# Kernel tuning notes

Measured on AMD Instinct MI355X. Metric: run time of the kernel, lower is better.

The kernel has to match this reference:

```python
import jax, jax.numpy as jnp
import numpy as np

B, T, D = 4, 2048, 1024
E, F, K = 8, 4096, 2  # num experts, ffn hidden, top-k


def setup_inputs() -> dict:
    key = jax.random.key(0)
    ks = jax.random.split(key, 7)
    s_in = 1.0 / np.sqrt(D)
    s_ff = 1.0 / np.sqrt(F)
    return {
        "x": jax.random.normal(ks[0], (B, T, D), dtype=jnp.float32),
        "Wg": jax.random.normal(ks[1], (D, E), dtype=jnp.float32) * s_in,
        "bg": jnp.zeros((E,), dtype=jnp.float32),
        "W1": jax.random.normal(ks[2], (E, D, F), dtype=jnp.float32) * s_in,
        "b1": jnp.zeros((E, F), dtype=jnp.float32),
        "W2": jax.random.normal(ks[3], (E, F, D), dtype=jnp.float32) * s_ff,
        "b2": jnp.zeros((E, D), dtype=jnp.float32),
    }


def reference(x, Wg, bg, W1, b1, W2, b2):
    # Gate: per-token expert logits [B, T, E]
    logits = jnp.einsum("btd,de->bte", x, Wg) + bg
    # Top-k per token, softmax over only the selected logits (as in the source)
    topv, topi = jax.lax.top_k(logits, K)          # [B, T, K]
    probs = jax.nn.softmax(topv, axis=-1)           # [B, T, K]
    out = jnp.zeros_like(x)
    # Loop over the small fixed expert set; each expert runs a dense MLP over
    # all tokens, masked/weighted by its routing probability (0 if unselected).
    for e in range(E):
        w = jnp.sum(probs * (topi == e), axis=-1)   # [B, T] combine weight
        h = jax.nn.gelu(jnp.einsum("btd,df->btf", x, W1[e]) + b1[e], approximate=False)
        y = jnp.einsum("btf,fd->btd", h, W2[e]) + b2[e]
        out = out + w[..., None] * y
    return out
```

## Files before the change

### kernel.cpp

```cpp
#include <hip/hip_runtime.h>
#include <cstdint>

#define B_ 4
#define T_ 2048
#define D_ 1024
#define E_ 8
#define F_ 4096
#define K_ 2
#define N_ (B_*T_)
#define NR_ (N_*K_)

#define TM 128
#define BK 64
#define MAXP (NR_ + E_*TM)
#define MAXMB (NR_/TM + E_)

typedef __attribute__((ext_vector_type(8))) short short8;
typedef __attribute__((ext_vector_type(4))) float f32x4;

typedef const __attribute__((address_space(1))) unsigned int* gp1_t;
typedef __attribute__((address_space(3))) unsigned int* lp3_t;

__device__ __forceinline__ void gl_lds16(const void* g, void* l) {
    __builtin_amdgcn_global_load_lds((gp1_t)g, (lp3_t)l, 16, 0, 0);
}

__device__ __forceinline__ unsigned short f2b(float f) {
    union { float f; unsigned int u; } v; v.f = f;
    unsigned int u = v.u;
    return (unsigned short)((u + 0x7FFFu + ((u >> 16) & 1u)) >> 16);
}

__device__ __forceinline__ float b2f(unsigned short u) {
    union { unsigned int i; float f; } v; v.i = ((unsigned int)u) << 16;
    return v.f;
}

__device__ __forceinline__ float gelu_exact(float x) {
    return 0.5f * x * (1.0f + erff(x * 0.70710678118654752440f));
}

__global__ __launch_bounds__(256) void gate_kernel(
    const float* __restrict__ x, const float* __restrict__ Wg,
    const float* __restrict__ bg, int* __restrict__ topi,
    float* __restrict__ topw, int* __restrict__ counts) {
    int tid  = threadIdx.x;
    int lane = tid & 63;
    int tok  = blockIdx.x * 4 + (tid >> 6);
    int e = lane & 7;
    int c = lane >> 3;
    const float4* xp = (const float4*)(x + (size_t)tok * D_ + c * 128);
    const float*  wp = Wg + (size_t)(c * 128) * E_ + e;
    float acc = 0.f;
    #pragma unroll 8
    for (int i = 0; i < 32; ++i) {
        float4 xv = xp[i];
        acc += xv.x * wp[(i*4+0)*E_];
        acc += xv.y * wp[(i*4+1)*E_];
        acc += xv.z * wp[(i*4+2)*E_];
        acc += xv.w * wp[(i*4+3)*E_];
    }
    acc += __shfl_xor(acc, 8, 64);
    acc += __shfl_xor(acc, 16, 64);
    acc += __shfl_xor(acc, 32, 64);
    float logit = acc + bg[e];
    float v1 = -3.4e38f, v2 = -3.4e38f; int i1 = -1, i2 = -1;
    for (int ee = 0; ee < 8; ++ee) {
        float le = __shfl(logit, ee, 64);
        if (le > v1) { v2 = v1; i2 = i1; v1 = le; i1 = ee; }
        else if (le > v2) { v2 = le; i2 = ee; }
    }
    if (lane == 0) {
        float p2 = expf(v2 - v1);
        float s  = 1.0f + p2;
        topi[tok*2]   = i1; topw[tok*2]   = 1.0f / s;
        topi[tok*2+1] = i2; topw[tok*2+1] = p2 / s;
        atomicAdd(&counts[i1], 1);
        atomicAdd(&counts[i2], 1);
    }
}

__global__ void scan_kernel(const int* __restrict__ counts,
                            int* __restrict__ offs, int* __restrict__ cursors,
                            int* __restrict__ mb_e, int* __restrict__ mb_m0) {
    if (threadIdx.x == 0) {
        int s = 0, mb = 0;
        for (int e = 0; e < E_; ++e) {
            offs[e] = s; cursors[e] = s;
            int nb = (counts[e] + TM - 1) / TM;
            for (int i = 0; i < nb; ++i) { mb_e[mb] = e; mb_m0[mb] = s + i*TM; ++mb; }
            s += nb * TM;
        }
        offs[E_] = s;
        for (int b = mb; b < MAXMB; ++b) mb_e[b] = -1;
    }
}

__global__ __launch_bounds__(256) void scatter_kernel(
    const int* __restrict__ topi, int* __restrict__ cursors,
    int* __restrict__ perm, int* __restrict__ slots) {
    int t = blockIdx.x * blockDim.x + threadIdx.x;
    if (t >= N_) return;
    #pragma unroll
    for (int k = 0; k < K_; ++k) {
        int e = topi[t*2 + k];
        int pos = atomicAdd(&cursors[e], 1);
        perm[pos] = t;
        slots[t*2 + k] = pos;
    }
}

__global__ __launch_bounds__(256) void castx_kernel(
    const float* __restrict__ x, unsigned short* __restrict__ xb) {
    int i = blockIdx.x * blockDim.x + threadIdx.x;
    float4 v = ((const float4*)x)[i];
    ushort4 o; o.x = f2b(v.x); o.y = f2b(v.y); o.z = f2b(v.z); o.w = f2b(v.w);
    ((ushort4*)xb)[i] = o;
}

__global__ __launch_bounds__(256) void tcast_kernel(
    const float* __restrict__ src, unsigned short* __restrict__ dst, int R, int C) {
    __shared__ float tile[64][65];
    int rb = blockIdx.x * 64, cb = blockIdx.y * 64;
    const float* s = src + (size_t)blockIdx.z * R * C;
    unsigned short* d = dst + (size_t)blockIdx.z * R * C;
    int tx = threadIdx.x & 15, ty = threadIdx.x >> 4;
    #pragma unroll
    for (int i = 0; i < 4; ++i) {
        int r = ty + i*16;
        float4 v = *(const float4*)&s[(size_t)(rb + r) * C + cb + tx*4];
        tile[r][tx*4+0] = v.x; tile[r][tx*4+1] = v.y;
        tile[r][tx*4+2] = v.z; tile[r][tx*4+3] = v.w;
    }
    __syncthreads();
    #pragma unroll
    for (int i = 0; i < 4; ++i) {
        int c = ty + i*16;
        ushort4 o;
        o.x = f2b(tile[tx*4+0][c]);
        o.y = f2b(tile[tx*4+1][c]);
        o.z = f2b(tile[tx*4+2][c]);
        o.w = f2b(tile[tx*4+3][c]);
        *(ushort4*)&d[(size_t)(cb + c) * R + rb + tx*4] = o;
    }
}

__global__ __launch_bounds__(256, 4) void ffn1_kernel(
    const unsigned short* __restrict__ Xb, const unsigned short* __restrict__ W1t,
    const float* __restrict__ b1, const int* __restrict__ perm,
    const int* __restrict__ mb_e, const int* __restrict__ mb_m0,
    unsigned short* __restrict__ H) {
    int e = mb_e[blockIdx.x];
    if (e < 0) return;
    int m0 = mb_m0[blockIdx.x];
    int n0 = blockIdx.y * 128;
    const unsigned short* Bw = W1t + (size_t)e * F_ * D_;

    __shared__ __align__(16) unsigned short lA[128*BK];
    __shared__ __align__(16) unsigned short lB[128*BK];

    int t = threadIdx.x;
    int lane = t & 63;
    int wv = t >> 6;
    int wrow = (wv >> 1) * 64, wcol = (wv & 1) * 64;
    int lr = lane & 15, q = lane >> 4;
    int xork = lr & 7;

    int sr = t >> 3;
    int sc = ((t & 7) ^ (sr & 7)) * 8;
    const unsigned short* pa[4];
    const unsigned short* pb[4];
    #pragma unroll
    for (int i = 0; i < 4; ++i) {
        int tok = perm[m0 + sr + 32*i];
        pa[i] = Xb + (size_t)tok * D_ + sc;
        pb[i] = Bw + (size_t)(n0 + sr + 32*i) * D_ + sc;
    }

    f32x4 acc[4][4];
    #pragma unroll
    for (int mi = 0; mi < 4; ++mi)
        #pragma unroll
        for (int ni = 0; ni < 4; ++ni)
            acc[mi][ni] = (f32x4){0.f, 0.f, 0.f, 0.f};

    for (int kk = 0; kk < D_/BK; ++kk) {
        int k0 = kk * BK;
        #pragma unroll
        for (int i = 0; i < 4; ++i) {
            gl_lds16(pa[i] + k0, &lA[i*2048 + t*8]);
            gl_lds16(pb[i] + k0, &lB[i*2048 + t*8]);
        }
        asm volatile("s_waitcnt vmcnt(0)" ::: "memory");
        __syncthreads();
        #pragma unroll
        for (int s = 0; s < 2; ++s) {
            short8 af[4], bf[4];
            #pragma unroll
            for (int mi = 0; mi < 4; ++mi)
                af[mi] = *(const short8*)&lA[(wrow + mi*16 + lr)*BK + (((s*4+q) ^ xork) * 8)];
            #pragma unroll
            for (int ni = 0; ni < 4; ++ni)
                bf[ni] = *(const short8*)&lB[(wcol + ni*16 + lr)*BK + (((s*4+q) ^ xork) * 8)];
            #pragma unroll
            for (int mi = 0; mi < 4; ++mi)
                #pragma unroll
                for (int ni = 0; ni < 4; ++ni)
                    acc[mi][ni] = __builtin_amdgcn_mfma_f32_16x16x32_bf16(
                        af[mi], bf[ni], acc[mi][ni], 0, 0, 0);
        }
        __syncthreads();
    }

    const float* b1e = b1 + (size_t)e * F_;
    #pragma unroll
    for (int mi = 0; mi < 4; ++mi) {
        int gr = m0 + wrow + mi*16 + q*4;
        #pragma unroll
        for (int ni = 0; ni < 4; ++ni) {
            int f = n0 + wcol + ni*16 + lr;
            float bb = b1e[f];
            #pragma unroll
            for (int r = 0; r < 4; ++r) {
                float h = gelu_exact(acc[mi][ni][r] + bb);
                H[(size_t)(gr + r) * F_ + f] = f2b(h);
            }
        }
    }
}

__global__ __launch_bounds__(256, 4) void ffn2_kernel(
    const unsigned short* __restrict__ H, const unsigned short* __restrict__ W2t,
    const float* __restrict__ b2,
    const int* __restrict__ mb_e, const int* __restrict__ mb_m0,
    unsigned short* __restrict__ Y) {
    int e = mb_e[blockIdx.x];
    if (e < 0) return;
    int m0 = mb_m0[blockIdx.x];
    int n0 = blockIdx.y * 128;
    const unsigned short* Bw = W2t + (size_t)e * D_ * F_;

    __shared__ __align__(16) unsigned short lA[128*BK];
    __shared__ __align__(16) unsigned short lB[128*BK];

    int t = threadIdx.x;
    int lane = t & 63;
    int wv = t >> 6;
    int wrow = (wv >> 1) * 64, wcol = (wv & 1) * 64;
    int lr = lane & 15, q = lane >> 4;
    int xork = lr & 7;

    int sr = t >> 3;
    int sc = ((t & 7) ^ (sr & 7)) * 8;
    const unsigned short* pa[4];
    const unsigned short* pb[4];
    #pragma unroll
    for (int i = 0; i < 4; ++i) {
        pa[i] = H  + (size_t)(m0 + sr + 32*i) * F_ + sc;
        pb[i] = Bw + (size_t)(n0 + sr + 32*i) * F_ + sc;
    }

    f32x4 acc[4][4];
    #pragma unroll
    for (int mi = 0; mi < 4; ++mi)
        #pragma unroll
        for (int ni = 0; ni < 4; ++ni)
            acc[mi][ni] = (f32x4){0.f, 0.f, 0.f, 0.f};

    for (int kk = 0; kk < F_/BK; ++kk) {
        int k0 = kk * BK;
        #pragma unroll
        for (int i = 0; i < 4; ++i) {
            gl_lds16(pa[i] + k0, &lA[i*2048 + t*8]);
            gl_lds16(pb[i] + k0, &lB[i*2048 + t*8]);
        }
        asm volatile("s_waitcnt vmcnt(0)" ::: "memory");
        __syncthreads();
        #pragma unroll
        for (int s = 0; s < 2; ++s) {
            short8 af[4], bf[4];
            #pragma unroll
            for (int mi = 0; mi < 4; ++mi)
                af[mi] = *(const short8*)&lA[(wrow + mi*16 + lr)*BK + (((s*4+q) ^ xork) * 8)];
            #pragma unroll
            for (int ni = 0; ni < 4; ++ni)
                bf[ni] = *(const short8*)&lB[(wcol + ni*16 + lr)*BK + (((s*4+q) ^ xork) * 8)];
            #pragma unroll
            for (int mi = 0; mi < 4; ++mi)
                #pragma unroll
                for (int ni = 0; ni < 4; ++ni)
                    acc[mi][ni] = __builtin_amdgcn_mfma_f32_16x16x32_bf16(
                        af[mi], bf[ni], acc[mi][ni], 0, 0, 0);
        }
        __syncthreads();
    }

    const float* b2e = b2 + (size_t)e * D_;
    #pragma unroll
    for (int mi = 0; mi < 4; ++mi) {
        int gr = m0 + wrow + mi*16 + q*4;
        #pragma unroll
        for (int ni = 0; ni < 4; ++ni) {
            int dcol = n0 + wcol + ni*16 + lr;
            float bb = b2e[dcol];
            #pragma unroll
            for (int r = 0; r < 4; ++r)
                Y[(size_t)(gr + r) * D_ + dcol] = f2b(acc[mi][ni][r] + bb);
        }
    }
}

__global__ __launch_bounds__(256) void combine_kernel(
    const unsigned short* __restrict__ Y, const int* __restrict__ slots,
    const float* __restrict__ topw, float* __restrict__ out) {
    int t  = blockIdx.x;
    int d4 = threadIdx.x * 4;
    int s0 = slots[t*2], s1 = slots[t*2+1];
    float w0 = topw[t*2], w1 = topw[t*2+1];
    ushort4 y0 = *(const ushort4*)&Y[(size_t)s0 * D_ + d4];
    ushort4 y1 = *(const ushort4*)&Y[(size_t)s1 * D_ + d4];
    float4 o;
    o.x = w0*b2f(y0.x) + w1*b2f(y1.x);
    o.y = w0*b2f(y0.y) + w1*b2f(y1.y);
    o.z = w0*b2f(y0.z) + w1*b2f(y1.z);
    o.w = w0*b2f(y0.w) + w1*b2f(y1.w);
    *(float4*)&out[(size_t)t * D_ + d4] = o;
}

extern "C" void kernel_launch(void* const* d_in, const int* in_sizes, int n_in,
                              void* d_out, int out_size, void* d_ws, size_t ws_size,
                              hipStream_t stream) {
    const float* x  = (const float*)d_in[0];
    const float* Wg = (const float*)d_in[1];
    const float* bg = (const float*)d_in[2];
    const float* W1 = (const float*)d_in[3];
    const float* b1 = (const float*)d_in[4];
    const float* W2 = (const float*)d_in[5];
    const float* b2 = (const float*)d_in[6];
    float* out = (float*)d_out;

    char* wsp = (char*)d_ws;
    size_t off = 0;
    auto alloc = [&](size_t bytes) {
        void* p = wsp + off;
        off += (bytes + 255) & ~(size_t)255;
        return p;
    };
    int*   topi    = (int*)  alloc((size_t)NR_*4);
    float* topw    = (float*)alloc((size_t)NR_*4);
    int*   slots   = (int*)  alloc((size_t)NR_*4);
    int*   counts  = (int*)  alloc(E_*4);
    int*   offs    = (int*)  alloc((E_+1)*4);
    int*   cursors = (int*)  alloc(E_*4);
    int*   mb_e    = (int*)  alloc(MAXMB*4);
    int*   mb_m0   = (int*)  alloc(MAXMB*4);
    int*   perm    = (int*)  alloc((size_t)MAXP*4);
    unsigned short* Xb  = (unsigned short*)alloc((size_t)N_*D_*2);
    unsigned short* W1t = (unsigned short*)alloc((size_t)E_*D_*F_*2);
    unsigned short* W2t = (unsigned short*)alloc((size_t)E_*D_*F_*2);
    unsigned short* Hb  = (unsigned short*)alloc((size_t)MAXP*F_*2);
    unsigned short* Yb  = (unsigned short*)alloc((size_t)MAXP*D_*2);

    hipMemsetAsync(counts, 0, E_*4, stream);
    hipMemsetAsync(perm, 0, (size_t)MAXP*4, stream);

    gate_kernel<<<N_/4, 256, 0, stream>>>(x, Wg, bg, topi, topw, counts);
    scan_kernel<<<1, 64, 0, stream>>>(counts, offs, cursors, mb_e, mb_m0);
    scatter_kernel<<<N_/256, 256, 0, stream>>>(topi, cursors, perm, slots);
    castx_kernel<<<(N_*(size_t)D_/4)/256, 256, 0, stream>>>(x, Xb);
    tcast_kernel<<<dim3(D_/64, F_/64, E_), 256, 0, stream>>>(W1, W1t, D_, F_);
    tcast_kernel<<<dim3(F_/64, D_/64, E_), 256, 0, stream>>>(W2, W2t, F_, D_);
    ffn1_kernel<<<dim3(MAXMB, F_/128), 256, 0, stream>>>(Xb, W1t, b1, perm, mb_e, mb_m0, Hb);
    ffn2_kernel<<<dim3(MAXMB, D_/128), 256, 0, stream>>>(Hb, W2t, b2, mb_e, mb_m0, Yb);
    combine_kernel<<<N_, 256, 0, stream>>>(Yb, slots, topw, out);
}
```

Baseline: 1.035 ms.

## Remap GEMM blocks per XCD for L2 expert-weight locality; warp-aggregate scatter atomics

The ffn1/ffn2 grids are remapped so that consecutive workgroup IDs, which round-robin across the 8 XCDs, give each XCD a contiguous range of M-blocks. Blocks of the same expert then tend to share an XCD's L2 and reuse its weight tiles instead of fetching them into every XCD's cache. The scatter kernel also replaces per-thread atomics with wave-level ballot aggregation, so each wave issues one atomic per expert. The remap assumes MAXMB is divisible by 8 and that the grid matches the original dimensions, and the order of tokens within each expert's rows changes.

```diff
diff --git a/kernel.cpp b/kernel.cpp
--- a/kernel.cpp
+++ b/kernel.cpp
@@ -14,6 +14,7 @@
 #define BK 64
 #define MAXP (NR_ + E_*TM)
 #define MAXMB (NR_/TM + E_)
+#define MBPX (MAXMB/8)
 
 typedef __attribute__((ext_vector_type(8))) short short8;
 typedef __attribute__((ext_vector_type(4))) float f32x4;
@@ -100,13 +101,31 @@
     const int* __restrict__ topi, int* __restrict__ cursors,
     int* __restrict__ perm, int* __restrict__ slots) {
     int t = blockIdx.x * blockDim.x + threadIdx.x;
-    if (t >= N_) return;
+    int lane = threadIdx.x & 63;
+    unsigned long long lanebit_m1 = (lane == 63) ? ~0ULL >> 1
+                                  : ((1ULL << (lane & 63)) - 1ULL);
+    lanebit_m1 = (1ULL << lane) - 1ULL;
     #pragma unroll
     for (int k = 0; k < K_; ++k) {
-        int e = topi[t*2 + k];
-        int pos = atomicAdd(&cursors[e], 1);
-        perm[pos] = t;
-        slots[t*2 + k] = pos;
+        int e = (t < N_) ? topi[t*2 + k] : -1;
+        int pos = 0;
+        #pragma unroll
+        for (int ee = 0; ee < E_; ++ee) {
+            unsigned long long mask = __ballot(e == ee);
+            if (mask) {
+                int leader = __ffsll((long long)mask) - 1;
+                int base = 0;
+                if (lane == leader)
+                    base = atomicAdd(&cursors[ee], __popcll(mask));
+                base = __shfl(base, leader, 64);
+                if (e == ee)
+                    pos = base + __popcll(mask & lanebit_m1);
+            }
+        }
+        if (t < N_) {
+            perm[pos] = t;
+            slots[t*2 + k] = pos;
+        }
     }
 }
 
@@ -150,10 +169,15 @@
     const float* __restrict__ b1, const int* __restrict__ perm,
     const int* __restrict__ mb_e, const int* __restrict__ mb_m0,
     unsigned short* __restrict__ H) {
-    int e = mb_e[blockIdx.x];
+    int o   = blockIdx.x + gridDim.x * blockIdx.y;
+    int xcd = o & 7;
+    int j   = o >> 3;
+    int mbi = xcd * MBPX + (j % MBPX);
+    int nbi = j / MBPX;
+    int e = mb_e[mbi];
     if (e < 0) return;
-    int m0 = mb_m0[blockIdx.x];
-    int n0 = blockIdx.y * 128;
+    int m0 = mb_m0[mbi];
+    int n0 = nbi * 128;
     const unsigned short* Bw = W1t + (size_t)e * F_ * D_;
 
     __shared__ __align__(16) unsigned short lA[128*BK];
@@ -234,10 +258,15 @@
     const float* __restrict__ b2,
     const int* __restrict__ mb_e, const int* __restrict__ mb_m0,
     unsigned short* __restrict__ Y) {
-    int e = mb_e[blockIdx.x];
+    int o   = blockIdx.x + gridDim.x * blockIdx.y;
+    int xcd = o & 7;
+    int j   = o >> 3;
+    int mbi = xcd * MBPX + (j % MBPX);
+    int nbi = j / MBPX;
+    int e = mb_e[mbi];
     if (e < 0) return;
-    int m0 = mb_m0[blockIdx.x];
-    int n0 = blockIdx.y * 128;
+    int m0 = mb_m0[mbi];
+    int n0 = nbi * 128;
     const unsigned short* Bw = W2t + (size_t)e * D_ * F_;
 
     __shared__ __align__(16) unsigned short lA[128*BK];
```

Result: faster. 946.9 us (-8.5%).
